# Kernel tuning notes

Hardware: AMD Instinct MI355X
Metric: run time of the kernel (lower is better)

The kernel has to match this reference:

```python
import jax, jax.numpy as jnp
import numpy as np

D_MODEL = 512
D_STATE = 16
D_CONV = 5
EXPAND = 2
HEADDIM = 64
D_INNER = EXPAND * D_MODEL            # 1024
NHEADS = D_INNER // HEADDIM           # 16
NGROUPS = 1
CONV_DIM = D_INNER + 2 * NGROUPS * D_STATE          # 1056
D_IN_PROJ = 2 * D_INNER + 2 * NGROUPS * D_STATE + NHEADS  # 2096
B_SZ, SEQ = 16, 960
EPS = 1e-5


def _mamba_params(key):
    ks = jax.random.split(key, 5)
    return dict(
        W_in=jax.random.normal(ks[0], (D_MODEL, D_IN_PROJ), jnp.float32) * 0.02,
        conv_w=jax.random.normal(ks[1], (CONV_DIM, D_CONV), jnp.float32) * 0.1,
        conv_b=jnp.zeros((CONV_DIM,), jnp.float32),
        dt_bias=jnp.log(jnp.expm1(jax.random.uniform(ks[2], (NHEADS,), jnp.float32, 0.001, 0.1))),
        A_log=jnp.log(jax.random.uniform(ks[3], (NHEADS,), jnp.float32, 1.0, 16.0)),
        D=jnp.ones((NHEADS,), jnp.float32),
        norm_w=jnp.ones((D_INNER,), jnp.float32),
        W_out=jax.random.normal(ks[4], (D_INNER, D_MODEL), jnp.float32) * 0.02,
    )


def setup_inputs() -> dict:
    key = jax.random.key(0)
    kx, kf, kb, kp = jax.random.split(key, 4)
    inp = {"x": jax.random.normal(kx, (B_SZ, SEQ, D_MODEL), jnp.float32)}
    for pref, k in (("fwd_", kf), ("bwd_", kb)):
        for n, v in _mamba_params(k).items():
            inp[pref + n] = v
    kp1, kp2 = jax.random.split(kp)
    inp["proj_W"] = jax.random.normal(kp1, (2 * D_MODEL, D_MODEL), jnp.float32) * 0.02
    inp["proj_b"] = jnp.zeros((D_MODEL,), jnp.float32)
    inp["ln_g"] = jnp.ones((D_MODEL,), jnp.float32)
    inp["ln_b"] = jnp.zeros((D_MODEL,), jnp.float32)
    return inp


def _mamba2(x, W_in, conv_w, conv_b, dt_bias, A_log, D, norm_w, W_out):
    """Mamba-2 block (mamba_ssm semantics): in_proj -> causal depthwise conv
    + silu -> selective SSM scan -> gated RMSNorm -> out_proj."""
    B, L, _ = x.shape
    zxbcdt = x @ W_in                                  # (B,L,2096)
    z = zxbcdt[..., :D_INNER]
    xBC = zxbcdt[..., D_INNER:D_INNER + CONV_DIM]
    dt = jax.nn.softplus(zxbcdt[..., D_INNER + CONV_DIM:] + dt_bias)  # (B,L,H)
    # causal depthwise conv over time
    xp = jnp.pad(xBC, ((0, 0), (D_CONV - 1, 0), (0, 0))).transpose(0, 2, 1)  # (B,C,Lp)
    xc = jax.lax.conv_general_dilated(
        xp, conv_w[:, None, :], window_strides=(1,), padding='VALID',
        dimension_numbers=('NCH', 'OIH', 'NCH'),
        feature_group_count=CONV_DIM).transpose(0, 2, 1)                  # (B,L,C)
    xBC = jax.nn.silu(xc + conv_b)
    xs = xBC[..., :D_INNER].reshape(B, L, NHEADS, HEADDIM)                # (B,L,H,P)
    Bm = xBC[..., D_INNER:D_INNER + D_STATE]                              # (B,L,N)
    Cm = xBC[..., D_INNER + D_STATE:]                                     # (B,L,N)
    A = -jnp.exp(A_log)                                                   # (H,)
    dA = jnp.exp(dt * A)                                                  # (B,L,H)
    dtx = dt[..., None] * xs                                              # (B,L,H,P)

    def step(h, inp):
        dA_t, dtx_t, B_t, C_t = inp
        # h: (B,H,P,N)
        h = h * dA_t[:, :, None, None] + jnp.einsum('bhp,bn->bhpn', dtx_t, B_t)
        y = jnp.einsum('bhpn,bn->bhp', h, C_t)
        return h, y

    h0 = jnp.zeros((B, NHEADS, HEADDIM, D_STATE), x.dtype)
    _, ys = jax.lax.scan(
        step, h0,
        (dA.transpose(1, 0, 2), dtx.transpose(1, 0, 2, 3),
         Bm.transpose(1, 0, 2), Cm.transpose(1, 0, 2)))
    y = ys.transpose(1, 0, 2, 3) + D[None, None, :, None] * xs            # (B,L,H,P)
    y = y.reshape(B, L, D_INNER)
    # gated RMSNorm (norm_before_gate=False)
    y = y * jax.nn.silu(z)
    y = y * jax.lax.rsqrt(jnp.mean(y * y, axis=-1, keepdims=True) + EPS) * norm_w
    return y @ W_out


def reference(x,
              fwd_W_in, fwd_conv_w, fwd_conv_b, fwd_dt_bias, fwd_A_log, fwd_D, fwd_norm_w, fwd_W_out,
              bwd_W_in, bwd_conv_w, bwd_conv_b, bwd_dt_bias, bwd_A_log, bwd_D, bwd_norm_w, bwd_W_out,
              proj_W, proj_b, ln_g, ln_b):
    x_f = _mamba2(x, fwd_W_in, fwd_conv_w, fwd_conv_b, fwd_dt_bias, fwd_A_log, fwd_D, fwd_norm_w, fwd_W_out)
    x_b = jnp.flip(_mamba2(jnp.flip(x, 1), bwd_W_in, bwd_conv_w, bwd_conv_b, bwd_dt_bias, bwd_A_log, bwd_D, bwd_norm_w, bwd_W_out), 1)
    x_out = jnp.concatenate([x_f, x_b], axis=-1) @ proj_W + proj_b
    h = x + x_out  # dropout is identity in eval
    mu = jnp.mean(h, axis=-1, keepdims=True)
    var = jnp.mean((h - mu) ** 2, axis=-1, keepdims=True)
    return (h - mu) * jax.lax.rsqrt(var + EPS) * ln_g + ln_b
```

## Files before the change

### kernel.cpp

```cpp
#include <hip/hip_runtime.h>
#include <hip/hip_bf16.h>

#define D_MODEL   512
#define D_STATE   16
#define D_CONV    5
#define HEADDIM   64
#define D_INNER   1024
#define NHEADS    16
#define CONV_DIM  1056
#define D_IN_PROJ 2096
#define B_SZ      16
#define SEQ       960
#define MROWS     (B_SZ*SEQ)
#define EPS       1e-5f
#define NCHUNK    6
#define CLEN      160

typedef __attribute__((ext_vector_type(8))) short   short8;
typedef __attribute__((ext_vector_type(8))) ushort  u16x8;
typedef __attribute__((ext_vector_type(4))) ushort  u16x4;
typedef __attribute__((ext_vector_type(4))) float   f32x4;

__device__ __forceinline__ ushort bf16_rne(float f) {
  union { float f; unsigned u; } x; x.f = f;
  unsigned u = x.u;
  return (ushort)((u + 0x7FFFu + ((u >> 16) & 1u)) >> 16);
}
__device__ __forceinline__ float bf16_f(ushort h) {
  union { unsigned u; float f; } x; x.u = ((unsigned)h) << 16;
  return x.f;
}
__device__ __forceinline__ void cvt_split(float v, ushort& h, ushort& l) {
  h = bf16_rne(v);
  l = bf16_rne(v - bf16_f(h));
}
#define CVT_SPLIT_V(F, HV, LV, I) do { ushort th_, tl_; \
    cvt_split((F), th_, tl_); HV[I] = th_; LV[I] = tl_; } while (0)

__global__ __launch_bounds__(256) void split_f32(
    const float* __restrict__ in, ushort* __restrict__ hi,
    ushort* __restrict__ lo, int n4)
{
  int i = blockIdx.x * 256 + threadIdx.x;
  if (i >= n4) return;
  float4 v = ((const float4*)in)[i];
  u16x4 h, l;
  CVT_SPLIT_V(v.x, h, l, 0);
  CVT_SPLIT_V(v.y, h, l, 1);
  CVT_SPLIT_V(v.z, h, l, 2);
  CVT_SPLIT_V(v.w, h, l, 3);
  ((u16x4*)hi)[i] = h;
  ((u16x4*)lo)[i] = l;
}

__global__ __launch_bounds__(256) void transpose_split(
    const float* __restrict__ in, ushort* __restrict__ oh,
    ushort* __restrict__ ol, int R, int C)
{
  __shared__ float t[32][33];
  int c0 = blockIdx.x * 32, r0 = blockIdx.y * 32;
  int tx = threadIdx.x & 31, ty = threadIdx.x >> 5;
  #pragma unroll
  for (int i = 0; i < 32; i += 8) {
    int r = r0 + ty + i, c = c0 + tx;
    t[ty + i][tx] = (r < R && c < C) ? in[(size_t)r * C + c] : 0.f;
  }
  __syncthreads();
  #pragma unroll
  for (int i = 0; i < 32; i += 8) {
    int c = c0 + ty + i, r = r0 + tx;
    if (c < C && r < R) {
      ushort h, l;
      cvt_split(t[tx][ty + i], h, l);
      oh[(size_t)c * R + r] = h;
      ol[(size_t)c * R + r] = l;
    }
  }
}

#define LDK 40

__global__ __launch_bounds__(256) void gemm_mfma_bf16(
    const ushort* __restrict__ Ah, const ushort* __restrict__ Al,
    const ushort* __restrict__ Bth, const ushort* __restrict__ Btl,
    float* __restrict__ C, const float* __restrict__ bias,
    int M, int N, int K, int lda, int ldb, int ldc, int accum)
{
  __shared__ ushort As_hi[128][LDK], As_lo[128][LDK];
  __shared__ ushort Bs_hi[128][LDK], Bs_lo[128][LDK];

  const int tid  = threadIdx.x;
  const int lane = tid & 63;
  const int wave = tid >> 6;
  const int wm   = wave >> 1;
  const int wn   = wave & 1;
  const int brow = blockIdx.x * 128;
  const int bcol = blockIdx.y * 128;

  const int sr = tid >> 1;
  const int sq = (tid & 1) * 16;

  f32x4 acc[4][4];
  #pragma unroll
  for (int i = 0; i < 4; ++i)
    #pragma unroll
    for (int j = 0; j < 4; ++j) acc[i][j] = f32x4{0.f, 0.f, 0.f, 0.f};

  const int fr = lane & 15;
  const int fk = (lane >> 4) * 8;

  for (int k0 = 0; k0 < K; k0 += 32) {
    {
      size_t off = (size_t)(brow + sr) * lda + k0 + sq;
      *(u16x8*)&As_hi[sr][sq]     = *(const u16x8*)&Ah[off];
      *(u16x8*)&As_hi[sr][sq + 8] = *(const u16x8*)&Ah[off + 8];
      *(u16x8*)&As_lo[sr][sq]     = *(const u16x8*)&Al[off];
      *(u16x8*)&As_lo[sr][sq + 8] = *(const u16x8*)&Al[off + 8];
    }
    {
      int n = bcol + sr;
      u16x8 z8 = {0,0,0,0,0,0,0,0};
      u16x8 h0 = z8, h1 = z8, l0 = z8, l1 = z8;
      if (n < N) {
        size_t off = (size_t)n * ldb + k0 + sq;
        h0 = *(const u16x8*)&Bth[off];
        h1 = *(const u16x8*)&Bth[off + 8];
        l0 = *(const u16x8*)&Btl[off];
        l1 = *(const u16x8*)&Btl[off + 8];
      }
      *(u16x8*)&Bs_hi[sr][sq]     = h0;
      *(u16x8*)&Bs_hi[sr][sq + 8] = h1;
      *(u16x8*)&Bs_lo[sr][sq]     = l0;
      *(u16x8*)&Bs_lo[sr][sq + 8] = l1;
    }
    __syncthreads();

    short8 ah[4], al[4], bh[4], bl[4];
    #pragma unroll
    for (int mf = 0; mf < 4; ++mf) {
      int r = wm * 64 + mf * 16 + fr;
      ah[mf] = *(const short8*)&As_hi[r][fk];
      al[mf] = *(const short8*)&As_lo[r][fk];
    }
    #pragma unroll
    for (int nf = 0; nf < 4; ++nf) {
      int n = wn * 64 + nf * 16 + fr;
      bh[nf] = *(const short8*)&Bs_hi[n][fk];
      bl[nf] = *(const short8*)&Bs_lo[n][fk];
    }
    #pragma unroll
    for (int mf = 0; mf < 4; ++mf)
      #pragma unroll
      for (int nf = 0; nf < 4; ++nf) {
        acc[mf][nf] = __builtin_amdgcn_mfma_f32_16x16x32_bf16(ah[mf], bh[nf], acc[mf][nf], 0, 0, 0);
        acc[mf][nf] = __builtin_amdgcn_mfma_f32_16x16x32_bf16(ah[mf], bl[nf], acc[mf][nf], 0, 0, 0);
        acc[mf][nf] = __builtin_amdgcn_mfma_f32_16x16x32_bf16(al[mf], bh[nf], acc[mf][nf], 0, 0, 0);
      }
    __syncthreads();
  }

  const int orow0 = brow + wm * 64 + ((lane >> 4) << 2);
  const int ocol0 = bcol + wn * 64 + fr;
  #pragma unroll
  for (int nf = 0; nf < 4; ++nf) {
    int col = ocol0 + nf * 16;
    if (col < N) {
      float bv = bias ? bias[col] : 0.f;
      #pragma unroll
      for (int mf = 0; mf < 4; ++mf) {
        #pragma unroll
        for (int j = 0; j < 4; ++j) {
          size_t idx = (size_t)(orow0 + mf * 16 + j) * ldc + col;
          float v = acc[mf][nf][j] + bv;
          if (accum) v += C[idx];
          C[idx] = v;
        }
      }
    }
  }
}

#define BM 128
#define BN 128
#define BKK 16

__global__ __launch_bounds__(256) void gemm_f32(
    const float* __restrict__ A, const float* __restrict__ B,
    float* __restrict__ C, const float* __restrict__ bias,
    int N, int K, int lda, int ldb, int ldc, int accum)
{
  __shared__ float As[BKK][BM + 4];
  __shared__ float Bs[BKK][BN + 4];

  const int tid = threadIdx.x;
  const int bm = blockIdx.x * BM;
  const int bn = blockIdx.y * BN;
  const int tx = tid & 15;
  const int ty = tid >> 4;

  const int am = tid >> 2;
  const int ak = (tid & 3) * 4;
  const int bk = tid >> 5;
  const int bc = (tid & 31) * 4;

  float acc[8][8];
  #pragma unroll
  for (int i = 0; i < 8; ++i)
    #pragma unroll
    for (int j = 0; j < 8; ++j) acc[i][j] = 0.f;

  const int colb = bn + bc;
  const bool bok = (colb < N);

  for (int k0 = 0; k0 < K; k0 += BKK) {
    float4 av0 = *(const float4*)&A[(size_t)(bm + am) * lda + k0 + ak];
    float4 av1 = *(const float4*)&A[(size_t)(bm + am + 64) * lda + k0 + ak];
    As[ak + 0][am]      = av0.x; As[ak + 1][am]      = av0.y;
    As[ak + 2][am]      = av0.z; As[ak + 3][am]      = av0.w;
    As[ak + 0][am + 64] = av1.x; As[ak + 1][am + 64] = av1.y;
    As[ak + 2][am + 64] = av1.z; As[ak + 3][am + 64] = av1.w;
    float4 z4 = make_float4(0.f, 0.f, 0.f, 0.f);
    float4 bv0 = bok ? *(const float4*)&B[(size_t)(k0 + bk) * ldb + colb]     : z4;
    float4 bv1 = bok ? *(const float4*)&B[(size_t)(k0 + bk + 8) * ldb + colb] : z4;
    *(float4*)&Bs[bk][bc]     = bv0;
    *(float4*)&Bs[bk + 8][bc] = bv1;
    __syncthreads();

    #pragma unroll
    for (int k = 0; k < BKK; ++k) {
      float4 a0 = *(const float4*)&As[k][ty * 4];
      float4 a1 = *(const float4*)&As[k][64 + ty * 4];
      float4 b0 = *(const float4*)&Bs[k][tx * 4];
      float4 b1 = *(const float4*)&Bs[k][64 + tx * 4];
      float a[8] = {a0.x, a0.y, a0.z, a0.w, a1.x, a1.y, a1.z, a1.w};
      float bb[8] = {b0.x, b0.y, b0.z, b0.w, b1.x, b1.y, b1.z, b1.w};
      #pragma unroll
      for (int i = 0; i < 8; ++i)
        #pragma unroll
        for (int j = 0; j < 8; ++j)
          acc[i][j] = __builtin_fmaf(a[i], bb[j], acc[i][j]);
    }
    __syncthreads();
  }

  const int n0 = bn + tx * 4;
  const int n1 = bn + 64 + tx * 4;
  float4 bias0 = make_float4(0.f, 0.f, 0.f, 0.f), bias1 = bias0;
  if (bias) {
    if (n0 < N) bias0 = *(const float4*)&bias[n0];
    if (n1 < N) bias1 = *(const float4*)&bias[n1];
  }
  #pragma unroll
  for (int i = 0; i < 8; ++i) {
    int row = bm + ((i < 4) ? (ty * 4 + i) : (64 + ty * 4 + i - 4));
    if (n0 < N) {
      float4 v = make_float4(acc[i][0] + bias0.x, acc[i][1] + bias0.y,
                             acc[i][2] + bias0.z, acc[i][3] + bias0.w);
      if (accum) {
        float4 c = *(const float4*)&C[(size_t)row * ldc + n0];
        v.x += c.x; v.y += c.y; v.z += c.z; v.w += c.w;
      }
      *(float4*)&C[(size_t)row * ldc + n0] = v;
    }
    if (n1 < N) {
      float4 v = make_float4(acc[i][4] + bias1.x, acc[i][5] + bias1.y,
                             acc[i][6] + bias1.z, acc[i][7] + bias1.w);
      if (accum) {
        float4 c = *(const float4*)&C[(size_t)row * ldc + n1];
        v.x += c.x; v.y += c.y; v.z += c.z; v.w += c.w;
      }
      *(float4*)&C[(size_t)row * ldc + n1] = v;
    }
  }
}

__global__ __launch_bounds__(256) void conv_silu(
    const float* __restrict__ zx, const float* __restrict__ cw,
    const float* __restrict__ cb, float* __restrict__ out, int dir)
{
  int idx = blockIdx.x * 256 + threadIdx.x;
  if (idx >= MROWS * CONV_DIM) return;
  int c  = idx % CONV_DIM;
  int bl = idx / CONV_DIM;
  int l  = bl % SEQ;
  int rowbase = bl - l;

  float acc = 0.f;
  #pragma unroll
  for (int j = 0; j < D_CONV; ++j) {
    int li = dir ? (l + 4 - j) : (l - 4 + j);
    if (li >= 0 && li < SEQ)
      acc = __builtin_fmaf(cw[c * D_CONV + j],
                           zx[(size_t)(rowbase + li) * D_IN_PROJ + D_INNER + c], acc);
  }
  float v = acc + cb[c];
  out[idx] = v / (1.f + __expf(-v));
}

__global__ __launch_bounds__(64) void scan_pass1(
    const float* __restrict__ zx, const float* __restrict__ xc,
    const float* __restrict__ dtb_p, const float* __restrict__ Alog_p,
    float* __restrict__ states, float* __restrict__ Pbuf, int dir)
{
  int blk = blockIdx.x;
  int c   = blk % NCHUNK;
  int bh  = blk / NCHUNK;
  int b = bh >> 4, hd = bh & 15;
  float dtb = dtb_p[hd];
  float A   = -__expf(Alog_p[hd]);
  int p = threadIdx.x;
  const float* xrow = xc + (size_t)b * SEQ * CONV_DIM;
  const float* zrow = zx + (size_t)b * SEQ * D_IN_PROJ;

  float h[16];
  #pragma unroll
  for (int n = 0; n < 16; ++n) h[n] = 0.f;
  float P = 1.f;

  const int s0 = c * CLEN, s1 = s0 + CLEN;

  float xv0, dtr0; float4 B0[4];
  float xv1, dtr1; float4 B1[4];

#define P1LOAD(ss, XV, DTR, BB) do {                                        \
    int tt_ = dir ? (SEQ - 1 - (ss)) : (ss);                                \
    size_t xb_ = (size_t)tt_ * CONV_DIM;                                    \
    XV  = xrow[xb_ + hd * 64 + p];                                          \
    DTR = zrow[(size_t)tt_ * D_IN_PROJ + (D_INNER + CONV_DIM) + hd];        \
    const float4* B4_ = (const float4*)(xrow + xb_ + D_INNER);              \
    BB[0] = B4_[0]; BB[1] = B4_[1]; BB[2] = B4_[2]; BB[3] = B4_[3];         \
  } while (0)

  P1LOAD(s0, xv0, dtr0, B0);
  P1LOAD(s0 + 1, xv1, dtr1, B1);

  #pragma unroll 4
  for (int s = s0; s < s1; ++s) {
    float dtrb = dtr0 + dtb;
    float dt = (dtrb > 20.f) ? dtrb : log1pf(__expf(dtrb));
    float dA = __expf(dt * A);
    P *= dA;
    float dtx = dt * xv0;
#define ST1(n, Bc) h[n] = __builtin_fmaf(h[n], dA, dtx * (Bc));
    ST1(0,  B0[0].x) ST1(1,  B0[0].y) ST1(2,  B0[0].z) ST1(3,  B0[0].w)
    ST1(4,  B0[1].x) ST1(5,  B0[1].y) ST1(6,  B0[1].z) ST1(7,  B0[1].w)
    ST1(8,  B0[2].x) ST1(9,  B0[2].y) ST1(10, B0[2].z) ST1(11, B0[2].w)
    ST1(12, B0[3].x) ST1(13, B0[3].y) ST1(14, B0[3].z) ST1(15, B0[3].w)
#undef ST1
    xv0 = xv1; dtr0 = dtr1;
    #pragma unroll
    for (int q = 0; q < 4; ++q) B0[q] = B1[q];
    int sn = s + 2; if (sn > s1 - 1) sn = s1 - 1;
    P1LOAD(sn, xv1, dtr1, B1);
  }
#undef P1LOAD

  float4* sp = (float4*)&states[(((size_t)bh * NCHUNK + c) * 64 + p) * 16];
  sp[0] = make_float4(h[0],  h[1],  h[2],  h[3]);
  sp[1] = make_float4(h[4],  h[5],  h[6],  h[7]);
  sp[2] = make_float4(h[8],  h[9],  h[10], h[11]);
  sp[3] = make_float4(h[12], h[13], h[14], h[15]);
  if (p == 0) Pbuf[bh * NCHUNK + c] = P;
}

__global__ __launch_bounds__(64) void scan_combine(
    float* __restrict__ states, const float* __restrict__ Pbuf)
{
  int bh = blockIdx.x;
  int p  = threadIdx.x;
  float4 h0 = make_float4(0,0,0,0), h1 = h0, h2 = h0, h3 = h0;
  for (int c = 0; c < NCHUNK; ++c) {
    float4* sp = (float4*)&states[(((size_t)bh * NCHUNK + c) * 64 + p) * 16];
    float P = Pbuf[bh * NCHUNK + c];
    float4 s0 = sp[0], s1 = sp[1], s2 = sp[2], s3 = sp[3];
    sp[0] = h0; sp[1] = h1; sp[2] = h2; sp[3] = h3;
    h0.x = __builtin_fmaf(P, h0.x, s0.x); h0.y = __builtin_fmaf(P, h0.y, s0.y);
    h0.z = __builtin_fmaf(P, h0.z, s0.z); h0.w = __builtin_fmaf(P, h0.w, s0.w);
    h1.x = __builtin_fmaf(P, h1.x, s1.x); h1.y = __builtin_fmaf(P, h1.y, s1.y);
    h1.z = __builtin_fmaf(P, h1.z, s1.z); h1.w = __builtin_fmaf(P, h1.w, s1.w);
    h2.x = __builtin_fmaf(P, h2.x, s2.x); h2.y = __builtin_fmaf(P, h2.y, s2.y);
    h2.z = __builtin_fmaf(P, h2.z, s2.z); h2.w = __builtin_fmaf(P, h2.w, s2.w);
    h3.x = __builtin_fmaf(P, h3.x, s3.x); h3.y = __builtin_fmaf(P, h3.y, s3.y);
    h3.z = __builtin_fmaf(P, h3.z, s3.z); h3.w = __builtin_fmaf(P, h3.w, s3.w);
  }
}

__global__ __launch_bounds__(64) void scan_pass3(
    const float* __restrict__ zx, const float* __restrict__ xc,
    const float* __restrict__ dtb_p, const float* __restrict__ Alog_p,
    const float* __restrict__ D_p, const float* __restrict__ states,
    float* __restrict__ y, int dir)
{
  int blk = blockIdx.x;
  int c   = blk % NCHUNK;
  int bh  = blk / NCHUNK;
  int b = bh >> 4, hd = bh & 15;
  float dtb = dtb_p[hd];
  float A   = -__expf(Alog_p[hd]);
  float Dv  = D_p[hd];
  int p = threadIdx.x;
  const float* xrow = xc + (size_t)b * SEQ * CONV_DIM;
  const float* zrow = zx + (size_t)b * SEQ * D_IN_PROJ;
  float*       yrow = y  + (size_t)b * SEQ * D_IN_PROJ + hd * 64 + p;

  float h[16];
  {
    const float4* sp =
        (const float4*)&states[(((size_t)bh * NCHUNK + c) * 64 + p) * 16];
    float4 s0 = sp[0], s1 = sp[1], s2 = sp[2], s3 = sp[3];
    h[0]=s0.x; h[1]=s0.y; h[2]=s0.z; h[3]=s0.w;
    h[4]=s1.x; h[5]=s1.y; h[6]=s1.z; h[7]=s1.w;
    h[8]=s2.x; h[9]=s2.y; h[10]=s2.z; h[11]=s2.w;
    h[12]=s3.x; h[13]=s3.y; h[14]=s3.z; h[15]=s3.w;
  }

  const int s0i = c * CLEN, s1i = s0i + CLEN;

  float xv0, zv0, dtr0; float4 B0[4], C0[4];
  float xv1, zv1, dtr1; float4 B1[4], C1[4];

#define P3LOAD(ss, XV, ZV, DTR, BB, CC) do {                                \
    int tt_ = dir ? (SEQ - 1 - (ss)) : (ss);                                \
    size_t xb_ = (size_t)tt_ * CONV_DIM;                                    \
    size_t zb_ = (size_t)tt_ * D_IN_PROJ;                                   \
    XV  = xrow[xb_ + hd * 64 + p];                                          \
    ZV  = zrow[zb_ + hd * 64 + p];                                          \
    DTR = zrow[zb_ + (D_INNER + CONV_DIM) + hd];                            \
    const float4* B4_ = (const float4*)(xrow + xb_ + D_INNER);              \
    const float4* C4_ = (const float4*)(xrow + xb_ + D_INNER + D_STATE);    \
    BB[0] = B4_[0]; BB[1] = B4_[1]; BB[2] = B4_[2]; BB[3] = B4_[3];         \
    CC[0] = C4_[0]; CC[1] = C4_[1]; CC[2] = C4_[2]; CC[3] = C4_[3];         \
  } while (0)

  P3LOAD(s0i, xv0, zv0, dtr0, B0, C0);
  P3LOAD(s0i + 1, xv1, zv1, dtr1, B1, C1);

  #pragma unroll 4
  for (int s = s0i; s < s1i; ++s) {
    int tt = dir ? (SEQ - 1 - s) : s;
    float dtrb = dtr0 + dtb;
    float dt = (dtrb > 20.f) ? dtrb : log1pf(__expf(dtrb));
    float dA = __expf(dt * A);
    float dtx = dt * xv0;
    float yv = 0.f;
#define ST3(n, Bc, Cc) \
    h[n] = __builtin_fmaf(h[n], dA, dtx * (Bc)); \
    yv = __builtin_fmaf(h[n], (Cc), yv);
    ST3(0,  B0[0].x, C0[0].x) ST3(1,  B0[0].y, C0[0].y)
    ST3(2,  B0[0].z, C0[0].z) ST3(3,  B0[0].w, C0[0].w)
    ST3(4,  B0[1].x, C0[1].x) ST3(5,  B0[1].y, C0[1].y)
    ST3(6,  B0[1].z, C0[1].z) ST3(7,  B0[1].w, C0[1].w)
    ST3(8,  B0[2].x, C0[2].x) ST3(9,  B0[2].y, C0[2].y)
    ST3(10, B0[2].z, C0[2].z) ST3(11, B0[2].w, C0[2].w)
    ST3(12, B0[3].x, C0[3].x) ST3(13, B0[3].y, C0[3].y)
    ST3(14, B0[3].z, C0[3].z) ST3(15, B0[3].w, C0[3].w)
#undef ST3

    float sz = zv0 / (1.f + __expf(-zv0));
    yrow[(size_t)tt * D_IN_PROJ] = (yv + Dv * xv0) * sz;

    xv0 = xv1; zv0 = zv1; dtr0 = dtr1;
    #pragma unroll
    for (int q = 0; q < 4; ++q) { B0[q] = B1[q]; C0[q] = C1[q]; }
    int sn = s + 2; if (sn > s1i - 1) sn = s1i - 1;
    P3LOAD(sn, xv1, zv1, dtr1, B1, C1);
  }
#undef P3LOAD
}

__device__ __forceinline__ float wave_sum64(float v) {
  #pragma unroll
  for (int off = 32; off; off >>= 1) v += __shfl_xor(v, off, 64);
  return v;
}

__global__ __launch_bounds__(256) void rmsnorm_split(
    const float* __restrict__ y, const float* __restrict__ w,
    ushort* __restrict__ yh, ushort* __restrict__ yl)
{
  int row = blockIdx.x;
  const float4* yp = (const float4*)(y + (size_t)row * D_IN_PROJ);
  int c = threadIdx.x;
  float4 v = yp[c];
  float ss = v.x * v.x + v.y * v.y + v.z * v.z + v.w * v.w;
  ss = wave_sum64(ss);
  __shared__ float part[4];
  if ((threadIdx.x & 63) == 0) part[threadIdx.x >> 6] = ss;
  __syncthreads();
  float tot = part[0] + part[1] + part[2] + part[3];
  float scale = rsqrtf(tot * (1.f / D_INNER) + EPS);
  float4 wv = ((const float4*)w)[c];
  u16x4 h, l;
  CVT_SPLIT_V(v.x * scale * wv.x, h, l, 0);
  CVT_SPLIT_V(v.y * scale * wv.y, h, l, 1);
  CVT_SPLIT_V(v.z * scale * wv.z, h, l, 2);
  CVT_SPLIT_V(v.w * scale * wv.w, h, l, 3);
  ((u16x4*)(yh + (size_t)row * D_INNER))[c] = h;
  ((u16x4*)(yl + (size_t)row * D_INNER))[c] = l;
}

__global__ __launch_bounds__(256) void ln_final(
    const float* __restrict__ x, const float* __restrict__ xo,
    const float* __restrict__ g, const float* __restrict__ bb,
    float* __restrict__ out)
{
  int row = blockIdx.x;
  int c = threadIdx.x;
  float2 xv = ((const float2*)(x  + (size_t)row * D_MODEL))[c];
  float2 ov = ((const float2*)(xo + (size_t)row * D_MODEL))[c];
  float hx = xv.x + ov.x, hy = xv.y + ov.y;
  float s  = hx + hy;
  float sq = hx * hx + hy * hy;
  s  = wave_sum64(s);
  sq = wave_sum64(sq);
  __shared__ float ps[4], pq[4];
  if ((threadIdx.x & 63) == 0) { ps[threadIdx.x >> 6] = s; pq[threadIdx.x >> 6] = sq; }
  __syncthreads();
  float tots = ps[0] + ps[1] + ps[2] + ps[3];
  float totq = pq[0] + pq[1] + pq[2] + pq[3];
  float mu  = tots * (1.f / D_MODEL);
  float var = totq * (1.f / D_MODEL) - mu * mu;
  float inv = rsqrtf(var + EPS);
  float2 gv = ((const float2*)g)[c];
  float2 bv = ((const float2*)bb)[c];
  float2 o;
  o.x = (hx - mu) * inv * gv.x + bv.x;
  o.y = (hy - mu) * inv * gv.y + bv.y;
  ((float2*)(out + (size_t)row * D_MODEL))[c] = o;
}

extern "C" void kernel_launch(void* const* d_in, const int* in_sizes, int n_in,
                              void* d_out, int out_size, void* d_ws, size_t ws_size,
                              hipStream_t stream) {
  const float* x      = (const float*)d_in[0];
  const float* proj_W = (const float*)d_in[17];
  const float* proj_b = (const float*)d_in[18];
  const float* ln_g   = (const float*)d_in[19];
  const float* ln_b   = (const float*)d_in[20];
  float* out = (float*)d_out;

  const size_t SZ_Z  = (size_t)MROWS * D_IN_PROJ;
  const size_t SZ_C  = (size_t)MROWS * CONV_DIM;
  const size_t SZ_W  = (size_t)D_INNER * D_MODEL;
  const size_t SZ_ST = (size_t)256 * NCHUNK * 64 * 16;
  const size_t SZ_P  = (size_t)256 * NCHUNK;
  const size_t SZ_SH = (SZ_ST + SZ_P > SZ_W) ? (SZ_ST + SZ_P) : SZ_W;
  const size_t NEED  = (SZ_Z + SZ_C + SZ_SH) * sizeof(float);
  if (ws_size < NEED) {
    (void)hipMemsetAsync(d_out, 0, (size_t)out_size * sizeof(float), stream);
    return;
  }
  float* zbuf    = (float*)d_ws;
  float* convbuf = zbuf + SZ_Z;
  float* shared  = convbuf + SZ_C;
  float* states  = shared;
  float* Pbuf    = shared + SZ_ST;
  float* ybuf    = zbuf + D_INNER;

  ushort* x_hi    = (ushort*)convbuf;
  ushort* x_lo    = x_hi + (size_t)MROWS * D_MODEL;
  ushort* WinT_hi = x_lo + (size_t)MROWS * D_MODEL;
  ushort* WinT_lo = WinT_hi + (size_t)D_IN_PROJ * D_MODEL;
  ushort* y_hi    = (ushort*)convbuf;
  ushort* y_lo    = y_hi + (size_t)MROWS * D_INNER;
  float*  Wcomb   = shared;
  ushort* WcT_hi  = (ushort*)(shared + SZ_W);
  ushort* WcT_lo  = WcT_hi + (size_t)D_MODEL * D_INNER;

  dim3 blk(256);

  for (int dir = 0; dir < 2; ++dir) {
    const float* W_in    = (const float*)d_in[dir ? 9  : 1];
    const float* conv_w  = (const float*)d_in[dir ? 10 : 2];
    const float* conv_b  = (const float*)d_in[dir ? 11 : 3];
    const float* dt_bias = (const float*)d_in[dir ? 12 : 4];
    const float* A_log   = (const float*)d_in[dir ? 13 : 5];
    const float* Dp      = (const float*)d_in[dir ? 14 : 6];
    const float* norm_w  = (const float*)d_in[dir ? 15 : 7];
    const float* W_out   = (const float*)d_in[dir ? 16 : 8];

    {
      int n4 = MROWS * D_MODEL / 4;
      split_f32<<<dim3((n4 + 255) / 256), blk, 0, stream>>>(x, x_hi, x_lo, n4);
    }
    transpose_split<<<dim3(66, 16), blk, 0, stream>>>(
        W_in, WinT_hi, WinT_lo, D_MODEL, D_IN_PROJ);

    gemm_mfma_bf16<<<dim3(MROWS / 128, 17), blk, 0, stream>>>(
        x_hi, x_lo, WinT_hi, WinT_lo, zbuf, nullptr,
        MROWS, D_IN_PROJ, D_MODEL, D_MODEL, D_MODEL, D_IN_PROJ, 0);

    {
      dim3 grid((MROWS * CONV_DIM + 255) / 256);
      conv_silu<<<grid, blk, 0, stream>>>(zbuf, conv_w, conv_b, convbuf, dir);
    }
    scan_pass1<<<dim3(256 * NCHUNK), dim3(64), 0, stream>>>(
        zbuf, convbuf, dt_bias, A_log, states, Pbuf, dir);
    scan_combine<<<dim3(256), dim3(64), 0, stream>>>(states, Pbuf);
    scan_pass3<<<dim3(256 * NCHUNK), dim3(64), 0, stream>>>(
        zbuf, convbuf, dt_bias, A_log, Dp, states, ybuf, dir);
    rmsnorm_split<<<dim3(MROWS), blk, 0, stream>>>(ybuf, norm_w, y_hi, y_lo);
    {
      dim3 grid(D_INNER / BM, (D_MODEL + BN - 1) / BN);
      gemm_f32<<<grid, blk, 0, stream>>>(
          W_out, proj_W + (size_t)dir * D_MODEL * D_MODEL, Wcomb, nullptr,
          D_MODEL, D_MODEL, D_MODEL, D_MODEL, D_MODEL, 0);
      transpose_split<<<dim3(16, 32), blk, 0, stream>>>(
          Wcomb, WcT_hi, WcT_lo, D_INNER, D_MODEL);
    }
    gemm_mfma_bf16<<<dim3(MROWS / 128, 4), blk, 0, stream>>>(
        y_hi, y_lo, WcT_hi, WcT_lo, out, dir ? nullptr : proj_b,
        MROWS, D_MODEL, D_INNER, D_INNER, D_INNER, D_MODEL, dir);
  }

  ln_final<<<dim3(MROWS), blk, 0, stream>>>(x, out, ln_g, ln_b, out);
}
```

Measured before the change: 1.348 ms.

## Use direct global-to-LDS loads in MFMA GEMM and raise scan chunk count

The split-bf16 GEMM now stages A/B hi/lo tiles with global_load_lds, writing straight into a fragment-ordered LDS layout so each lane reads its MFMA operand with one contiguous 16-byte load. This drops the register round trip and the padded-row layout. Separately, the chunked SSM scan takes the chunk count at runtime and picks 20 chunks when the workspace allows, which gives more parallel blocks and shorter serial chunks at the cost of a longer combine pass. Out-of-range B rows are now clamped rather than zeroed, which relies on those output columns being masked at store time.

```diff
diff --git a/kernel.cpp b/kernel.cpp
--- a/kernel.cpp
+++ b/kernel.cpp
@@ -13,8 +13,6 @@
 #define SEQ       960
 #define MROWS     (B_SZ*SEQ)
 #define EPS       1e-5f
-#define NCHUNK    6
-#define CLEN      160
 
 typedef __attribute__((ext_vector_type(8))) short   short8;
 typedef __attribute__((ext_vector_type(8))) ushort  u16x8;
@@ -36,6 +34,12 @@
 }
 #define CVT_SPLIT_V(F, HV, LV, I) do { ushort th_, tl_; \
     cvt_split((F), th_, tl_); HV[I] = th_; LV[I] = tl_; } while (0)
+
+__device__ __forceinline__ void gload16(const ushort* g, ushort* l) {
+  __builtin_amdgcn_global_load_lds(
+      (const __attribute__((address_space(1))) void*)g,
+      (__attribute__((address_space(3))) void*)l, 16, 0, 0);
+}
 
 __global__ __launch_bounds__(256) void split_f32(
     const float* __restrict__ in, ushort* __restrict__ hi,
@@ -78,16 +82,13 @@
   }
 }
 
-#define LDK 40
-
 __global__ __launch_bounds__(256) void gemm_mfma_bf16(
-    const ushort* __restrict__ Ah, const ushort* __restrict__ Al,
-    const ushort* __restrict__ Bth, const ushort* __restrict__ Btl,
+    const ushort* __restrict__ Ah, size_t loA,
+    const ushort* __restrict__ Bth, size_t loB,
     float* __restrict__ C, const float* __restrict__ bias,
     int M, int N, int K, int lda, int ldb, int ldc, int accum)
 {
-  __shared__ ushort As_hi[128][LDK], As_lo[128][LDK];
-  __shared__ ushort Bs_hi[128][LDK], Bs_lo[128][LDK];
+  __shared__ ushort lds[16384];
 
   const int tid  = threadIdx.x;
   const int lane = tid & 63;
@@ -97,8 +98,20 @@
   const int brow = blockIdx.x * 128;
   const int bcol = blockIdx.y * 128;
 
-  const int sr = tid >> 1;
-  const int sq = (tid & 1) * 16;
+  const int fr  = lane & 15;
+  const int kg8 = ((lane >> 4) & 3) * 8;
+
+  const int srow0 = (wave * 2 + 0) * 16 + fr;
+  const int srow1 = (wave * 2 + 1) * 16 + fr;
+  int bn0 = bcol + srow0; if (bn0 > N - 1) bn0 = N - 1;
+  int bn1 = bcol + srow1; if (bn1 > N - 1) bn1 = N - 1;
+  const ushort* pA0 = Ah  + (size_t)(brow + srow0) * lda + kg8;
+  const ushort* pA1 = Ah  + (size_t)(brow + srow1) * lda + kg8;
+  const ushort* pB0 = Bth + (size_t)bn0 * ldb + kg8;
+  const ushort* pB1 = Bth + (size_t)bn1 * ldb + kg8;
+
+  const int ld0 = wave * 1024;
+  const int ld1 = wave * 1024 + 512;
 
   f32x4 acc[4][4];
   #pragma unroll
@@ -106,47 +119,26 @@
     #pragma unroll
     for (int j = 0; j < 4; ++j) acc[i][j] = f32x4{0.f, 0.f, 0.f, 0.f};
 
-  const int fr = lane & 15;
-  const int fk = (lane >> 4) * 8;
-
   for (int k0 = 0; k0 < K; k0 += 32) {
-    {
-      size_t off = (size_t)(brow + sr) * lda + k0 + sq;
-      *(u16x8*)&As_hi[sr][sq]     = *(const u16x8*)&Ah[off];
-      *(u16x8*)&As_hi[sr][sq + 8] = *(const u16x8*)&Ah[off + 8];
-      *(u16x8*)&As_lo[sr][sq]     = *(const u16x8*)&Al[off];
-      *(u16x8*)&As_lo[sr][sq + 8] = *(const u16x8*)&Al[off + 8];
-    }
-    {
-      int n = bcol + sr;
-      u16x8 z8 = {0,0,0,0,0,0,0,0};
-      u16x8 h0 = z8, h1 = z8, l0 = z8, l1 = z8;
-      if (n < N) {
-        size_t off = (size_t)n * ldb + k0 + sq;
-        h0 = *(const u16x8*)&Bth[off];
-        h1 = *(const u16x8*)&Bth[off + 8];
-        l0 = *(const u16x8*)&Btl[off];
-        l1 = *(const u16x8*)&Btl[off + 8];
-      }
-      *(u16x8*)&Bs_hi[sr][sq]     = h0;
-      *(u16x8*)&Bs_hi[sr][sq + 8] = h1;
-      *(u16x8*)&Bs_lo[sr][sq]     = l0;
-      *(u16x8*)&Bs_lo[sr][sq + 8] = l1;
-    }
+    gload16(pA0,        &lds[ld0]);
+    gload16(pA1,        &lds[ld1]);
+    gload16(pA0 + loA,  &lds[4096 + ld0]);
+    gload16(pA1 + loA,  &lds[4096 + ld1]);
+    gload16(pB0,        &lds[8192 + ld0]);
+    gload16(pB1,        &lds[8192 + ld1]);
+    gload16(pB0 + loB,  &lds[12288 + ld0]);
+    gload16(pB1 + loB,  &lds[12288 + ld1]);
     __syncthreads();
 
     short8 ah[4], al[4], bh[4], bl[4];
     #pragma unroll
-    for (int mf = 0; mf < 4; ++mf) {
-      int r = wm * 64 + mf * 16 + fr;
-      ah[mf] = *(const short8*)&As_hi[r][fk];
-      al[mf] = *(const short8*)&As_lo[r][fk];
-    }
-    #pragma unroll
-    for (int nf = 0; nf < 4; ++nf) {
-      int n = wn * 64 + nf * 16 + fr;
-      bh[nf] = *(const short8*)&Bs_hi[n][fk];
-      bl[nf] = *(const short8*)&Bs_lo[n][fk];
+    for (int f = 0; f < 4; ++f) {
+      int amfg = wm * 4 + f;
+      int bnfg = wn * 4 + f;
+      ah[f] = *(const short8*)&lds[amfg * 512 + lane * 8];
+      al[f] = *(const short8*)&lds[4096 + amfg * 512 + lane * 8];
+      bh[f] = *(const short8*)&lds[8192 + bnfg * 512 + lane * 8];
+      bl[f] = *(const short8*)&lds[12288 + bnfg * 512 + lane * 8];
     }
     #pragma unroll
     for (int mf = 0; mf < 4; ++mf)
@@ -157,6 +149,8 @@
         acc[mf][nf] = __builtin_amdgcn_mfma_f32_16x16x32_bf16(al[mf], bh[nf], acc[mf][nf], 0, 0, 0);
       }
     __syncthreads();
+
+    pA0 += 32; pA1 += 32; pB0 += 32; pB1 += 32;
   }
 
   const int orow0 = brow + wm * 64 + ((lane >> 4) << 2);
@@ -300,11 +294,12 @@
 __global__ __launch_bounds__(64) void scan_pass1(
     const float* __restrict__ zx, const float* __restrict__ xc,
     const float* __restrict__ dtb_p, const float* __restrict__ Alog_p,
-    float* __restrict__ states, float* __restrict__ Pbuf, int dir)
+    float* __restrict__ states, float* __restrict__ Pbuf, int dir,
+    int nchunk, int clen)
 {
   int blk = blockIdx.x;
-  int c   = blk % NCHUNK;
-  int bh  = blk / NCHUNK;
+  int c   = blk % nchunk;
+  int bh  = blk / nchunk;
   int b = bh >> 4, hd = bh & 15;
   float dtb = dtb_p[hd];
   float A   = -__expf(Alog_p[hd]);
@@ -317,7 +312,7 @@
   for (int n = 0; n < 16; ++n) h[n] = 0.f;
   float P = 1.f;
 
-  const int s0 = c * CLEN, s1 = s0 + CLEN;
+  const int s0 = c * clen, s1 = s0 + clen;
 
   float xv0, dtr0; float4 B0[4];
   float xv1, dtr1; float4 B1[4];
@@ -355,23 +350,23 @@
   }
 #undef P1LOAD
 
-  float4* sp = (float4*)&states[(((size_t)bh * NCHUNK + c) * 64 + p) * 16];
+  float4* sp = (float4*)&states[(((size_t)bh * nchunk + c) * 64 + p) * 16];
   sp[0] = make_float4(h[0],  h[1],  h[2],  h[3]);
   sp[1] = make_float4(h[4],  h[5],  h[6],  h[7]);
   sp[2] = make_float4(h[8],  h[9],  h[10], h[11]);
   sp[3] = make_float4(h[12], h[13], h[14], h[15]);
-  if (p == 0) Pbuf[bh * NCHUNK + c] = P;
+  if (p == 0) Pbuf[bh * nchunk + c] = P;
 }
 
 __global__ __launch_bounds__(64) void scan_combine(
-    float* __restrict__ states, const float* __restrict__ Pbuf)
+    float* __restrict__ states, const float* __restrict__ Pbuf, int nchunk)
 {
   int bh = blockIdx.x;
   int p  = threadIdx.x;
   float4 h0 = make_float4(0,0,0,0), h1 = h0, h2 = h0, h3 = h0;
-  for (int c = 0; c < NCHUNK; ++c) {
-    float4* sp = (float4*)&states[(((size_t)bh * NCHUNK + c) * 64 + p) * 16];
-    float P = Pbuf[bh * NCHUNK + c];
+  for (int c = 0; c < nchunk; ++c) {
+    float4* sp = (float4*)&states[(((size_t)bh * nchunk + c) * 64 + p) * 16];
+    float P = Pbuf[bh * nchunk + c];
     float4 s0 = sp[0], s1 = sp[1], s2 = sp[2], s3 = sp[3];
     sp[0] = h0; sp[1] = h1; sp[2] = h2; sp[3] = h3;
     h0.x = __builtin_fmaf(P, h0.x, s0.x); h0.y = __builtin_fmaf(P, h0.y, s0.y);
@@ -389,11 +384,11 @@
     const float* __restrict__ zx, const float* __restrict__ xc,
     const float* __restrict__ dtb_p, const float* __restrict__ Alog_p,
     const float* __restrict__ D_p, const float* __restrict__ states,
-    float* __restrict__ y, int dir)
+    float* __restrict__ y, int dir, int nchunk, int clen)
 {
   int blk = blockIdx.x;
-  int c   = blk % NCHUNK;
-  int bh  = blk / NCHUNK;
+  int c   = blk % nchunk;
+  int bh  = blk / nchunk;
   int b = bh >> 4, hd = bh & 15;
   float dtb = dtb_p[hd];
   float A   = -__expf(Alog_p[hd]);
@@ -406,7 +401,7 @@
   float h[16];
   {
     const float4* sp =
-        (const float4*)&states[(((size_t)bh * NCHUNK + c) * 64 + p) * 16];
+        (const float4*)&states[(((size_t)bh * nchunk + c) * 64 + p) * 16];
     float4 s0 = sp[0], s1 = sp[1], s2 = sp[2], s3 = sp[3];
     h[0]=s0.x; h[1]=s0.y; h[2]=s0.z; h[3]=s0.w;
     h[4]=s1.x; h[5]=s1.y; h[6]=s1.z; h[7]=s1.w;
@@ -414,7 +409,7 @@
     h[12]=s3.x; h[13]=s3.y; h[14]=s3.z; h[15]=s3.w;
   }
 
-  const int s0i = c * CLEN, s1i = s0i + CLEN;
+  const int s0i = c * clen, s1i = s0i + clen;
 
   float xv0, zv0, dtr0; float4 B0[4], C0[4];
   float xv1, zv1, dtr1; float4 B1[4], C1[4];
@@ -539,17 +534,26 @@
   const float* ln_b   = (const float*)d_in[20];
   float* out = (float*)d_out;
 
-  const size_t SZ_Z  = (size_t)MROWS * D_IN_PROJ;
-  const size_t SZ_C  = (size_t)MROWS * CONV_DIM;
-  const size_t SZ_W  = (size_t)D_INNER * D_MODEL;
-  const size_t SZ_ST = (size_t)256 * NCHUNK * 64 * 16;
-  const size_t SZ_P  = (size_t)256 * NCHUNK;
-  const size_t SZ_SH = (SZ_ST + SZ_P > SZ_W) ? (SZ_ST + SZ_P) : SZ_W;
-  const size_t NEED  = (SZ_Z + SZ_C + SZ_SH) * sizeof(float);
-  if (ws_size < NEED) {
+  const size_t SZ_Z    = (size_t)MROWS * D_IN_PROJ;
+  const size_t SZ_C    = (size_t)MROWS * CONV_DIM;
+  const size_t SZ_W    = (size_t)D_INNER * D_MODEL;
+  const size_t SZ_POST = SZ_W + (size_t)D_MODEL * D_INNER;
+  int nchunk = 0;
+  {
+    const int cand[3] = {20, 12, 6};
+    for (int i = 0; i < 3 && !nchunk; ++i) {
+      size_t st = (size_t)256 * cand[i] * 64 * 16 + (size_t)256 * cand[i];
+      size_t sh = st > SZ_POST ? st : SZ_POST;
+      if (ws_size >= (SZ_Z + SZ_C + sh) * sizeof(float)) nchunk = cand[i];
+    }
+  }
+  if (!nchunk) {
     (void)hipMemsetAsync(d_out, 0, (size_t)out_size * sizeof(float), stream);
     return;
   }
+  const int clen = SEQ / nchunk;
+  const size_t SZ_ST = (size_t)256 * nchunk * 64 * 16;
+
   float* zbuf    = (float*)d_ws;
   float* convbuf = zbuf + SZ_Z;
   float* shared  = convbuf + SZ_C;
@@ -558,14 +562,18 @@
   float* ybuf    = zbuf + D_INNER;
 
   ushort* x_hi    = (ushort*)convbuf;
-  ushort* x_lo    = x_hi + (size_t)MROWS * D_MODEL;
-  ushort* WinT_hi = x_lo + (size_t)MROWS * D_MODEL;
-  ushort* WinT_lo = WinT_hi + (size_t)D_IN_PROJ * D_MODEL;
+  const size_t loX = (size_t)MROWS * D_MODEL;
+  ushort* x_lo    = x_hi + loX;
+  ushort* WinT_hi = x_lo + loX;
+  const size_t loWin = (size_t)D_IN_PROJ * D_MODEL;
+  ushort* WinT_lo = WinT_hi + loWin;
   ushort* y_hi    = (ushort*)convbuf;
-  ushort* y_lo    = y_hi + (size_t)MROWS * D_INNER;
+  const size_t loY = (size_t)MROWS * D_INNER;
+  ushort* y_lo    = y_hi + loY;
   float*  Wcomb   = shared;
   ushort* WcT_hi  = (ushort*)(shared + SZ_W);
-  ushort* WcT_lo  = WcT_hi + (size_t)D_MODEL * D_INNER;
+  const size_t loWc = (size_t)D_MODEL * D_INNER;
+  ushort* WcT_lo  = WcT_hi + loWc;
 
   dim3 blk(256);
 
@@ -587,18 +595,18 @@
         W_in, WinT_hi, WinT_lo, D_MODEL, D_IN_PROJ);
 
     gemm_mfma_bf16<<<dim3(MROWS / 128, 17), blk, 0, stream>>>(
-        x_hi, x_lo, WinT_hi, WinT_lo, zbuf, nullptr,
+        x_hi, loX, WinT_hi, loWin, zbuf, nullptr,
         MROWS, D_IN_PROJ, D_MODEL, D_MODEL, D_MODEL, D_IN_PROJ, 0);
 
     {
       dim3 grid((MROWS * CONV_DIM + 255) / 256);
       conv_silu<<<grid, blk, 0, stream>>>(zbuf, conv_w, conv_b, convbuf, dir);
     }
-    scan_pass1<<<dim3(256 * NCHUNK), dim3(64), 0, stream>>>(
-        zbuf, convbuf, dt_bias, A_log, states, Pbuf, dir);
-    scan_combine<<<dim3(256), dim3(64), 0, stream>>>(states, Pbuf);
-    scan_pass3<<<dim3(256 * NCHUNK), dim3(64), 0, stream>>>(
-        zbuf, convbuf, dt_bias, A_log, Dp, states, ybuf, dir);
+    scan_pass1<<<dim3(256 * nchunk), dim3(64), 0, stream>>>(
+        zbuf, convbuf, dt_bias, A_log, states, Pbuf, dir, nchunk, clen);
+    scan_combine<<<dim3(256), dim3(64), 0, stream>>>(states, Pbuf, nchunk);
+    scan_pass3<<<dim3(256 * nchunk), dim3(64), 0, stream>>>(
+        zbuf, convbuf, dt_bias, A_log, Dp, states, ybuf, dir, nchunk, clen);
     rmsnorm_split<<<dim3(MROWS), blk, 0, stream>>>(ybuf, norm_w, y_hi, y_lo);
     {
       dim3 grid(D_INNER / BM, (D_MODEL + BN - 1) / BN);
@@ -609,7 +617,7 @@
           Wcomb, WcT_hi, WcT_lo, D_INNER, D_MODEL);
     }
     gemm_mfma_bf16<<<dim3(MROWS / 128, 4), blk, 0, stream>>>(
-        y_hi, y_lo, WcT_hi, WcT_lo, out, dir ? nullptr : proj_b,
+        y_hi, loY, WcT_hi, loWc, out, dir ? nullptr : proj_b,
         MROWS, D_MODEL, D_INNER, D_INNER, D_INNER, D_MODEL, dir);
   }
 
```

Measured after the change: 1.294 ms. 1.04x faster.
